# Kernel tuning notes

Measured on AMD Instinct MI355X. Metric: run time of the kernel, lower is better.

Reference implementation:

```python
import jax, jax.numpy as jnp
import numpy as np

N = 50000      # nodes
E = 800000     # edges
F_IN = 1284    # nfeat (hardcoded in module)
H = 128        # hidden_layers
NEG_SLOPE_ATT = 0.2   # PyG GATConv default
NEG_SLOPE_OUT = 0.01  # CustomLeakyReLU assumed default


def setup_inputs() -> dict:
    key = jax.random.key(0)
    ks = jax.random.split(key, 16)
    def glorot(k, shape):
        fan = sum(shape) if len(shape) > 1 else shape[0] + 1
        lim = np.sqrt(6.0 / fan).astype(np.float32)
        return jax.random.uniform(k, shape, jnp.float32, -lim, lim)
    x = jax.random.normal(ks[0], (N, F_IN), jnp.float32)
    edge_index = jax.random.randint(ks[1], (2, E), 0, N, jnp.int64)
    edge_attr = jax.random.uniform(ks[2], (E, 1), jnp.float32)
    return {
        'x': x, 'edge_index': edge_index, 'edge_attr': edge_attr,
        # conv1: 1284 -> 128, heads=1, edge_dim=1
        'W1': glorot(ks[3], (F_IN, H)),
        'att_src1': glorot(ks[4], (H,)),
        'att_dst1': glorot(ks[5], (H,)),
        'We1': glorot(ks[6], (1, H)),
        'att_e1': glorot(ks[7], (H,)),
        'b1': jnp.zeros((H,), jnp.float32),
        # conv2: 128 -> 1, heads=1, edge_dim=1
        'W2': glorot(ks[8], (H, 1)),
        'att_src2': glorot(ks[9], (1,)),
        'att_dst2': glorot(ks[10], (1,)),
        'We2': glorot(ks[11], (1, 1)),
        'att_e2': glorot(ks[12], (1,)),
        'b2': jnp.zeros((1,), jnp.float32),
    }


def _gat_layer(h_in, src, dst, eattr, W, a_src, a_dst, We, a_e, b):
    # h_in: [N, Fin]; src/dst: [E'] (with self-loops); eattr: [E', 1]
    h = h_in @ W                                   # [N, F]
    alpha_src = h @ a_src                          # [N]
    alpha_dst = h @ a_dst                          # [N]
    alpha_e = (eattr @ We) @ a_e                   # [E']
    alpha = alpha_src[src] + alpha_dst[dst] + alpha_e
    alpha = jax.nn.leaky_relu(alpha, NEG_SLOPE_ATT)
    # segment softmax over destination neighborhoods
    m = jax.ops.segment_max(alpha, dst, num_segments=N)
    ea = jnp.exp(alpha - m[dst])
    denom = jax.ops.segment_sum(ea, dst, num_segments=N)
    coef = ea / (denom[dst] + 1e-16)               # [E']
    out = jax.ops.segment_sum(coef[:, None] * h[src], dst, num_segments=N)
    return out + b


def reference(x, edge_index, edge_attr, W1, att_src1, att_dst1, We1, att_e1, b1,
              W2, att_src2, att_dst2, We2, att_e2, b2):
    # add self loops (PyG default, fill_value='mean' for edge_attr)
    loop = jnp.arange(N, dtype=edge_index.dtype)
    src = jnp.concatenate([edge_index[0], loop])
    dst = jnp.concatenate([edge_index[1], loop])
    loop_attr = jnp.broadcast_to(jnp.mean(edge_attr, axis=0, keepdims=True), (N, 1))
    eattr = jnp.concatenate([edge_attr, loop_attr], axis=0)

    x1 = _gat_layer(x, src, dst, eattr, W1, att_src1, att_dst1, We1, att_e1, b1)
    x2 = jax.nn.elu(x1)
    # dropout p=0.2 is identity in eval mode
    x4 = _gat_layer(x2, src, dst, eattr, W2, att_src2, att_dst2, We2, att_e2, b2)
    return jax.nn.leaky_relu(x4, NEG_SLOPE_OUT)  # [N, 1]
```

## Files before the change

kernel.cpp:

```cpp
#include <hip/hip_runtime.h>
#include <math.h>

#define NN 50000
#define NE 800000
#define NEP 850000
#define FI 1284
#define HD 128
#define KP 1312
#define NSTEP 41
#define NH (NN * HD)
#define PAD 64
#define NBLK ((NN + 255) / 256)
#define NROWB ((NN + 127) / 128)
#define WP_ELEMS (NSTEP * 4096)
#define WT_BLKS ((WP_ELEMS + 255) / 256)

typedef float f32x4 __attribute__((ext_vector_type(4)));
typedef short bfrag __attribute__((ext_vector_type(8)));


__device__ __forceinline__ float wave_reduce_sum(float v) {
    #pragma unroll
    for (int off = 32; off; off >>= 1) v += __shfl_down(v, off);
    return v;
}

__device__ __forceinline__ ushort f2bf(float f) {
    unsigned u = __float_as_uint(f);
    u += 0x7FFFu + ((u >> 16) & 1u);
    return (ushort)(u >> 16);
}

__device__ __forceinline__ float bf2f(ushort u) {
    return __uint_as_float(((unsigned)u) << 16);
}

__device__ __forceinline__ ushort f2h(float f) {
    _Float16 h = (_Float16)f;
    return *(ushort*)&h;
}

__device__ __forceinline__ float h2f(ushort u) {
    _Float16 h = *(_Float16*)&u;
    return (float)h;
}

__device__ __forceinline__ bfrag cvt_frag(float4 a0, float4 a1) {
    union { int i[4]; bfrag f; } u;
    asm("v_cvt_pk_bf16_f32 %0, %1, %2" : "=v"(u.i[0]) : "v"(a0.x), "v"(a0.y));
    asm("v_cvt_pk_bf16_f32 %0, %1, %2" : "=v"(u.i[1]) : "v"(a0.z), "v"(a0.w));
    asm("v_cvt_pk_bf16_f32 %0, %1, %2" : "=v"(u.i[2]) : "v"(a1.x), "v"(a1.y));
    asm("v_cvt_pk_bf16_f32 %0, %1, %2" : "=v"(u.i[3]) : "v"(a1.z), "v"(a1.w));
    return u.f;
}


__global__ __launch_bounds__(256) void k_pre_a(int* cursor, float* sc,
                                               const float* We1, const float* ae1,
                                               const float* We2, const float* ae2) {
    if (blockIdx.x < NBLK) {
        int i = blockIdx.x * 256 + threadIdx.x;
        if (i < NN) cursor[i] = i * PAD;
        if (i == 0) { sc[0] = 0.f; sc[3] = 0.f; sc[4] = 0.f; sc[5] = 0.f; sc[6] = 0.f; sc[7] = 0.f; }
    } else if (threadIdx.x < 64) {
        int l = threadIdx.x;
        float v = We1[l] * ae1[l] + We1[l + 64] * ae1[l + 64];
        v = wave_reduce_sum(v);
        if (l == 0) { sc[1] = v; sc[2] = We2[0] * ae2[0]; }
    }
}


__global__ __launch_bounds__(256) void k_pre_b(const float* __restrict__ W, ushort* __restrict__ Wp,
                                               const float* __restrict__ eattr, float* sc) {
    int b = blockIdx.x;
    if (b < WT_BLKS) {
        int i = b * 256 + threadIdx.x;
        if (i >= WP_ELEMS) return;
        int s = i >> 12;
        int r = i & 4095;
        int cg = r >> 9;
        int q = r & 511;
        int lane = q >> 3, j = q & 7;
        int k = s * 32 + (lane >> 4) * 8 + j;
        int c = cg * 16 + (lane & 15);
        float v = (k < FI) ? W[(size_t)k * HD + c] : 0.f;
        Wp[i] = f2bf(v);
    } else {
        __shared__ float wsum[4];
        int b2 = b - WT_BLKS;
        float v = 0.f;
        for (int i = b2 * 256 + threadIdx.x; i < NE; i += 256 * 256)
            v += eattr[i];
        v = wave_reduce_sum(v);
        int wid = threadIdx.x >> 6, l = threadIdx.x & 63;
        if (l == 0) wsum[wid] = v;
        __syncthreads();
        if (threadIdx.x == 0)
            atomicAdd(&sc[0], wsum[0] + wsum[1] + wsum[2] + wsum[3]);
    }
}


__global__ __launch_bounds__(512) void k_gemm1_mfma(const float* __restrict__ x,
                                                    const ushort* __restrict__ Wp,
                                                    ushort* __restrict__ h1,
                                                    const float* __restrict__ asrc,
                                                    const float* __restrict__ adst,
                                                    float* __restrict__ as1,
                                                    float* __restrict__ ad1) {
    __shared__ float  As[3][128][32];
    __shared__ ushort Bs[3][4096];
    const int t = threadIdx.x;
    const int wid = t >> 6, l = t & 63;
    const int lr = l & 15, lg = l >> 4;
    const int wrow0 = blockIdx.x * 128 + wid * 16;

    const int srow = l >> 3;
    const int schunk = (l & 7) ^ srow;
    int g0 = wrow0 + srow;      if (g0 > NN - 1) g0 = NN - 1;
    int g1 = wrow0 + 8 + srow;  if (g1 > NN - 1) g1 = NN - 1;
    const float* sp0 = x + (size_t)g0 * FI + schunk * 4;
    const float* sp1 = x + (size_t)g1 * FI + schunk * 4;

    const ushort* bq0 = Wp + wid * 512 + l * 8;

    const int rs0 = (lg * 2)     ^ (lr & 7);
    const int rs1 = (lg * 2 + 1) ^ (lr & 7);

    f32x4 acc[8];
    #pragma unroll
    for (int c = 0; c < 8; ++c) acc[c] = (f32x4){0.f, 0.f, 0.f, 0.f};

#define STAGE(B, IT) do { \
    __builtin_amdgcn_global_load_lds( \
        (const __attribute__((address_space(1))) unsigned int*)(sp0 + (size_t)(IT) * 32), \
        (__attribute__((address_space(3))) unsigned int*)&As[B][wid * 16][0], 16, 0, 0); \
    __builtin_amdgcn_global_load_lds( \
        (const __attribute__((address_space(1))) unsigned int*)(sp1 + (size_t)(IT) * 32), \
        (__attribute__((address_space(3))) unsigned int*)&As[B][wid * 16 + 8][0], 16, 0, 0); \
    __builtin_amdgcn_global_load_lds( \
        (const __attribute__((address_space(1))) unsigned int*)(bq0 + (size_t)(IT) * 4096), \
        (__attribute__((address_space(3))) unsigned int*)&Bs[B][wid * 512], 16, 0, 0); \
} while (0)

    STAGE(0, 0);
    STAGE(1, 1);
    STAGE(2, 2);
    asm volatile("s_waitcnt vmcnt(6)" ::: "memory");
    __builtin_amdgcn_s_barrier();

    int bsel = 0;
    for (int it = 0; it < 40; ++it) {
        bfrag bfr[8];
        #pragma unroll
        for (int cg = 0; cg < 8; ++cg)
            bfr[cg] = *(const bfrag*)&Bs[bsel][cg * 512 + l * 8];

        float4 a0 = *(const float4*)&As[bsel][wid * 16 + lr][rs0 * 4];
        float4 a1 = *(const float4*)&As[bsel][wid * 16 + lr][rs1 * 4];
        bfrag af = cvt_frag(a0, a1);
        #pragma unroll
        for (int cg = 0; cg < 8; ++cg)
            acc[cg] = __builtin_amdgcn_mfma_f32_16x16x32_bf16(af, bfr[cg], acc[cg], 0, 0, 0);

        __builtin_amdgcn_s_barrier();
        if (it + 3 < 40) {
            STAGE(bsel, it + 3);
            asm volatile("s_waitcnt vmcnt(6)" ::: "memory");
        } else if (it == 37) {
            asm volatile("s_waitcnt vmcnt(3)" ::: "memory");
        } else if (it == 38) {
            asm volatile("s_waitcnt vmcnt(0)" ::: "memory");
        }
        __builtin_amdgcn_s_barrier();
        bsel = (bsel == 2) ? 0 : bsel + 1;
    }
#undef STAGE

    {
        int rowc = wrow0 + lr; if (rowc > NN - 1) rowc = NN - 1;
        float4 a0t = make_float4(0.f, 0.f, 0.f, 0.f);
        if (lg == 0) a0t = *(const float4*)(x + (size_t)rowc * FI + 1280);
        bfrag af;
        af[0] = (short)f2bf(a0t.x); af[1] = (short)f2bf(a0t.y);
        af[2] = (short)f2bf(a0t.z); af[3] = (short)f2bf(a0t.w);
        af[4] = 0; af[5] = 0; af[6] = 0; af[7] = 0;
        const ushort* wqs = Wp + (size_t)40 * 4096 + l * 8;
        #pragma unroll
        for (int cg = 0; cg < 8; ++cg) {
            bfrag bf = *(const bfrag*)(wqs + cg * 512);
            acc[cg] = __builtin_amdgcn_mfma_f32_16x16x32_bf16(af, bf, acc[cg], 0, 0, 0);
        }
    }

    #pragma unroll
    for (int cg = 0; cg < 8; ++cg) {
        #pragma unroll
        for (int r = 0; r < 4; ++r) {
            int gr = wrow0 + lg * 4 + r;
            if (gr < NN) h1[(size_t)gr * HD + cg * 16 + lr] = f2bf(acc[cg][r]);
        }
    }

    float av[8], dv[8];
    #pragma unroll
    for (int cg = 0; cg < 8; ++cg) {
        av[cg] = asrc[cg * 16 + lr];
        dv[cg] = adst[cg * 16 + lr];
    }
    #pragma unroll
    for (int r = 0; r < 4; ++r) {
        float s = 0.f, d = 0.f;
        #pragma unroll
        for (int cg = 0; cg < 8; ++cg) {
            s += acc[cg][r] * av[cg];
            d += acc[cg][r] * dv[cg];
        }
        #pragma unroll
        for (int off = 1; off < 16; off <<= 1) {
            s += __shfl_xor(s, off);
            d += __shfl_xor(d, off);
        }
        int gr = wrow0 + lg * 4 + r;
        if (lr == 0 && gr < NN) { as1[gr] = s; ad1[gr] = d; }
    }
}


__global__ void k_place(const int* __restrict__ ei, const float* __restrict__ eattr,
                        const float* __restrict__ sc,
                        const float* __restrict__ as1, const float* __restrict__ ad1,
                        int* cursor, int2* __restrict__ csr) {
    int e = blockIdx.x * blockDim.x + threadIdx.x;
    if (e >= NEP) return;
    int s, d; float av;
    if (e < NE) { s = ei[e]; d = ei[NE + e]; av = eattr[e]; }
    else        { s = d = e - NE; av = sc[0] * (1.0f / NE); }
    float a = as1[s] + ad1[d] + sc[1] * av;
    a = (a > 0.f) ? a : 0.2f * a;
    int pos = atomicAdd(&cursor[d], 1);
    if (pos - d * PAD < PAD)
        csr[pos] = make_int2(s, ((int)f2h(a) << 16) | (int)f2h(av));
}


__global__ __launch_bounds__(256) void k_layer1(const int2* __restrict__ csr,
                                                const int* __restrict__ cursor,
                                                const ushort* __restrict__ h1,
                                                const float* __restrict__ b1,
                                                const float* __restrict__ W2,
                                                float* __restrict__ h2) {
    int wid = threadIdx.x >> 6, l = threadIdx.x & 63;
    int d = blockIdx.x * 4 + wid;
    if (d >= NN) return;
    int s0 = d * PAD;
    int n = cursor[d] - s0; if (n > PAD) n = PAD;

    float m = -INFINITY;
    for (int i = 0; i < n; ++i)
        m = fmaxf(m, h2f((ushort)(csr[s0 + i].y >> 16)));

    float den = 0.f, ax = 0.f, ay = 0.f;
    int i = 0;
    for (; i + 4 <= n; i += 4) {
        int2 e0 = csr[s0 + i],     e1 = csr[s0 + i + 1];
        int2 e2 = csr[s0 + i + 2], e3 = csr[s0 + i + 3];
        float w0 = expf(h2f((ushort)(e0.y >> 16)) - m);
        float w1 = expf(h2f((ushort)(e1.y >> 16)) - m);
        float w2 = expf(h2f((ushort)(e2.y >> 16)) - m);
        float w3 = expf(h2f((ushort)(e3.y >> 16)) - m);
        ushort2 hv0 = *(const ushort2*)&h1[(size_t)e0.x * HD + 2 * l];
        ushort2 hv1 = *(const ushort2*)&h1[(size_t)e1.x * HD + 2 * l];
        ushort2 hv2 = *(const ushort2*)&h1[(size_t)e2.x * HD + 2 * l];
        ushort2 hv3 = *(const ushort2*)&h1[(size_t)e3.x * HD + 2 * l];
        den += w0 + w1 + w2 + w3;
        ax += w0 * bf2f(hv0.x) + w1 * bf2f(hv1.x) + w2 * bf2f(hv2.x) + w3 * bf2f(hv3.x);
        ay += w0 * bf2f(hv0.y) + w1 * bf2f(hv1.y) + w2 * bf2f(hv2.y) + w3 * bf2f(hv3.y);
    }
    for (; i < n; ++i) {
        int2 e0 = csr[s0 + i];
        float w0 = expf(h2f((ushort)(e0.y >> 16)) - m);
        ushort2 hv0 = *(const ushort2*)&h1[(size_t)e0.x * HD + 2 * l];
        den += w0;
        ax += w0 * bf2f(hv0.x);
        ay += w0 * bf2f(hv0.y);
    }
    float inv = 1.f / (den + 1e-16f);
    ax *= inv; ay *= inv;
    float2 bb = *(const float2*)&b1[2 * l];
    float2 w  = *(const float2*)&W2[2 * l];
    float a = ax + bb.x; a = (a > 0.f) ? a : (expf(a) - 1.f);
    float b = ay + bb.y; b = (b > 0.f) ? b : (expf(b) - 1.f);
    float p = a * w.x + b * w.y;
    p = wave_reduce_sum(p);
    if (l == 0) h2[d] = p;
}


__global__ __launch_bounds__(256) void k_layer2(const int2* __restrict__ csr,
                                                const int* __restrict__ cursor,
                                                const float* __restrict__ h2,
                                                const float* __restrict__ as2,
                                                const float* __restrict__ ad2,
                                                const float* __restrict__ sc,
                                                const float* __restrict__ b2,
                                                float* __restrict__ out) {
    int d = blockIdx.x * blockDim.x + threadIdx.x;
    if (d >= NN) return;
    int s0 = d * PAD;
    int n = cursor[d] - s0; if (n > PAD) n = PAD;
    float A = as2[0], D = ad2[0], c2 = sc[2];
    float hd = D * h2[d];

    float m = -INFINITY;
    for (int i = 0; i < n; ++i) {
        int2 sa = csr[s0 + i];
        float a = A * h2[sa.x] + hd + c2 * h2f((ushort)(sa.y & 0xFFFF));
        a = (a > 0.f) ? a : 0.2f * a;
        m = fmaxf(m, a);
    }
    float den = 0.f, num = 0.f;
    for (int i = 0; i < n; ++i) {
        int2 sa = csr[s0 + i];
        float hs = h2[sa.x];
        float a = A * hs + hd + c2 * h2f((ushort)(sa.y & 0xFFFF));
        a = (a > 0.f) ? a : 0.2f * a;
        float wgt = expf(a - m);
        den += wgt;
        num += wgt * hs;
    }
    float v = num / (den + 1e-16f) + b2[0];
    out[d] = (v >= 0.f) ? v : 0.01f * v;
}


extern "C" void kernel_launch(void* const* d_in, const int* in_sizes, int n_in,
                              void* d_out, int out_size, void* d_ws, size_t ws_size,
                              hipStream_t stream) {
    const float* x     = (const float*)d_in[0];
    const int*   ei    = (const int*)d_in[1];
    const float* eattr = (const float*)d_in[2];
    const float* W1    = (const float*)d_in[3];
    const float* asrc1 = (const float*)d_in[4];
    const float* adst1 = (const float*)d_in[5];
    const float* We1   = (const float*)d_in[6];
    const float* ae1   = (const float*)d_in[7];
    const float* b1    = (const float*)d_in[8];
    const float* W2    = (const float*)d_in[9];
    const float* as2   = (const float*)d_in[10];
    const float* ad2   = (const float*)d_in[11];
    const float* We2   = (const float*)d_in[12];
    const float* ae2   = (const float*)d_in[13];
    const float* b2    = (const float*)d_in[14];
    float* out = (float*)d_out;

    ushort* h1  = (ushort*)d_ws;
    float* as1  = (float*)(h1 + (size_t)NH);
    float* ad1  = as1 + NN;
    float* h2   = ad1 + NN;
    float* sc   = h2 + NN;
    int*   cursor = (int*)(sc + 8);
    int2*  csr    = (int2*)(cursor + NN);
    ushort* Wp  = (ushort*)(csr + (size_t)NN * PAD);

    k_pre_a<<<NBLK + 1, 256, 0, stream>>>(cursor, sc, We1, ae1, We2, ae2);
    k_pre_b<<<WT_BLKS + 256, 256, 0, stream>>>(W1, Wp, eattr, sc);

    k_gemm1_mfma<<<NROWB, 512, 0, stream>>>(x, Wp, h1, asrc1, adst1, as1, ad1);

    k_place<<<(NEP + 255) / 256, 256, 0, stream>>>(ei, eattr, sc, as1, ad1, cursor, csr);

    k_layer1<<<(NN + 3) / 4, 256, 0, stream>>>(csr, cursor, h1, b1, W2, h2);
    k_layer2<<<(NN + 255) / 256, 256, 0, stream>>>(csr, cursor, h2, as2, ad2, sc, b2, out);
}
```

Baseline: 223.5 us.

## Merge preprocessing kernels and use online softmax in aggregation layers

The two preprocessing kernels become one launch. The edge-attribute sum is now written as per-block partials, and a single wave in the GEMM kernel reduces them, which removes the atomic and the separate zeroing. Both aggregation kernels switch from a two-pass max-then-sum softmax to a single-pass online softmax with rescaling, so each CSR segment is read once instead of twice. The cost is extra exp and rescale work whenever the running max grows, plus a small serial reduction at the start of GEMM block 0.

```diff
diff --git a/kernel.cpp b/kernel.cpp
--- a/kernel.cpp
+++ b/kernel.cpp
@@ -55,27 +55,24 @@
 }
 
 
-__global__ __launch_bounds__(256) void k_pre_a(int* cursor, float* sc,
-                                               const float* We1, const float* ae1,
-                                               const float* We2, const float* ae2) {
-    if (blockIdx.x < NBLK) {
-        int i = blockIdx.x * 256 + threadIdx.x;
+__global__ __launch_bounds__(256) void k_pre(int* cursor, float* sc,
+                                             const float* We1, const float* ae1,
+                                             const float* We2, const float* ae2,
+                                             const float* __restrict__ W, ushort* __restrict__ Wp,
+                                             const float* __restrict__ eattr, float* bsum) {
+    int b = blockIdx.x;
+    if (b < NBLK) {
+        int i = b * 256 + threadIdx.x;
         if (i < NN) cursor[i] = i * PAD;
-        if (i == 0) { sc[0] = 0.f; sc[3] = 0.f; sc[4] = 0.f; sc[5] = 0.f; sc[6] = 0.f; sc[7] = 0.f; }
-    } else if (threadIdx.x < 64) {
-        int l = threadIdx.x;
-        float v = We1[l] * ae1[l] + We1[l + 64] * ae1[l + 64];
-        v = wave_reduce_sum(v);
-        if (l == 0) { sc[1] = v; sc[2] = We2[0] * ae2[0]; }
-    }
-}
-
-
-__global__ __launch_bounds__(256) void k_pre_b(const float* __restrict__ W, ushort* __restrict__ Wp,
-                                               const float* __restrict__ eattr, float* sc) {
-    int b = blockIdx.x;
-    if (b < WT_BLKS) {
-        int i = b * 256 + threadIdx.x;
+    } else if (b == NBLK) {
+        if (threadIdx.x < 64) {
+            int l = threadIdx.x;
+            float v = We1[l] * ae1[l] + We1[l + 64] * ae1[l + 64];
+            v = wave_reduce_sum(v);
+            if (l == 0) { sc[1] = v; sc[2] = We2[0] * ae2[0]; }
+        }
+    } else if (b < NBLK + 1 + WT_BLKS) {
+        int i = (b - NBLK - 1) * 256 + threadIdx.x;
         if (i >= WP_ELEMS) return;
         int s = i >> 12;
         int r = i & 4095;
@@ -88,7 +85,7 @@
         Wp[i] = f2bf(v);
     } else {
         __shared__ float wsum[4];
-        int b2 = b - WT_BLKS;
+        int b2 = b - NBLK - 1 - WT_BLKS;
         float v = 0.f;
         for (int i = b2 * 256 + threadIdx.x; i < NE; i += 256 * 256)
             v += eattr[i];
@@ -97,7 +94,7 @@
         if (l == 0) wsum[wid] = v;
         __syncthreads();
         if (threadIdx.x == 0)
-            atomicAdd(&sc[0], wsum[0] + wsum[1] + wsum[2] + wsum[3]);
+            bsum[b2] = wsum[0] + wsum[1] + wsum[2] + wsum[3];
     }
 }
 
@@ -108,13 +105,21 @@
                                                     const float* __restrict__ asrc,
                                                     const float* __restrict__ adst,
                                                     float* __restrict__ as1,
-                                                    float* __restrict__ ad1) {
+                                                    float* __restrict__ ad1,
+                                                    const float* __restrict__ bsum,
+                                                    float* sc) {
     __shared__ float  As[3][128][32];
     __shared__ ushort Bs[3][4096];
     const int t = threadIdx.x;
     const int wid = t >> 6, l = t & 63;
     const int lr = l & 15, lg = l >> 4;
     const int wrow0 = blockIdx.x * 128 + wid * 16;
+
+    if (blockIdx.x == 0 && wid == 0) {
+        float v = bsum[l] + bsum[l + 64] + bsum[l + 128] + bsum[l + 192];
+        v = wave_reduce_sum(v);
+        if (l == 0) sc[0] = v;
+    }
 
     const int srow = l >> 3;
     const int schunk = (l & 7) ^ srow;
@@ -257,31 +262,39 @@
     int s0 = d * PAD;
     int n = cursor[d] - s0; if (n > PAD) n = PAD;
 
-    float m = -INFINITY;
-    for (int i = 0; i < n; ++i)
-        m = fmaxf(m, h2f((ushort)(csr[s0 + i].y >> 16)));
-
-    float den = 0.f, ax = 0.f, ay = 0.f;
+    float m = -INFINITY, den = 0.f, ax = 0.f, ay = 0.f;
     int i = 0;
     for (; i + 4 <= n; i += 4) {
         int2 e0 = csr[s0 + i],     e1 = csr[s0 + i + 1];
         int2 e2 = csr[s0 + i + 2], e3 = csr[s0 + i + 3];
-        float w0 = expf(h2f((ushort)(e0.y >> 16)) - m);
-        float w1 = expf(h2f((ushort)(e1.y >> 16)) - m);
-        float w2 = expf(h2f((ushort)(e2.y >> 16)) - m);
-        float w3 = expf(h2f((ushort)(e3.y >> 16)) - m);
+        float a0 = h2f((ushort)(e0.y >> 16));
+        float a1 = h2f((ushort)(e1.y >> 16));
+        float a2 = h2f((ushort)(e2.y >> 16));
+        float a3 = h2f((ushort)(e3.y >> 16));
         ushort2 hv0 = *(const ushort2*)&h1[(size_t)e0.x * HD + 2 * l];
         ushort2 hv1 = *(const ushort2*)&h1[(size_t)e1.x * HD + 2 * l];
         ushort2 hv2 = *(const ushort2*)&h1[(size_t)e2.x * HD + 2 * l];
         ushort2 hv3 = *(const ushort2*)&h1[(size_t)e3.x * HD + 2 * l];
+        float mt = fmaxf(fmaxf(a0, a1), fmaxf(a2, a3));
+        if (mt > m) {
+            float r = expf(m - mt);
+            den *= r; ax *= r; ay *= r; m = mt;
+        }
+        float w0 = expf(a0 - m), w1 = expf(a1 - m);
+        float w2 = expf(a2 - m), w3 = expf(a3 - m);
         den += w0 + w1 + w2 + w3;
         ax += w0 * bf2f(hv0.x) + w1 * bf2f(hv1.x) + w2 * bf2f(hv2.x) + w3 * bf2f(hv3.x);
         ay += w0 * bf2f(hv0.y) + w1 * bf2f(hv1.y) + w2 * bf2f(hv2.y) + w3 * bf2f(hv3.y);
     }
     for (; i < n; ++i) {
         int2 e0 = csr[s0 + i];
-        float w0 = expf(h2f((ushort)(e0.y >> 16)) - m);
+        float a0 = h2f((ushort)(e0.y >> 16));
         ushort2 hv0 = *(const ushort2*)&h1[(size_t)e0.x * HD + 2 * l];
+        if (a0 > m) {
+            float r = expf(m - a0);
+            den *= r; ax *= r; ay *= r; m = a0;
+        }
+        float w0 = expf(a0 - m);
         den += w0;
         ax += w0 * bf2f(hv0.x);
         ay += w0 * bf2f(hv0.y);
@@ -313,19 +326,39 @@
     float A = as2[0], D = ad2[0], c2 = sc[2];
     float hd = D * h2[d];
 
-    float m = -INFINITY;
-    for (int i = 0; i < n; ++i) {
-        int2 sa = csr[s0 + i];
-        float a = A * h2[sa.x] + hd + c2 * h2f((ushort)(sa.y & 0xFFFF));
-        a = (a > 0.f) ? a : 0.2f * a;
-        m = fmaxf(m, a);
-    }
-    float den = 0.f, num = 0.f;
-    for (int i = 0; i < n; ++i) {
+    float m = -INFINITY, den = 0.f, num = 0.f;
+    int i = 0;
+    for (; i + 4 <= n; i += 4) {
+        int2 s_0 = csr[s0 + i],     s_1 = csr[s0 + i + 1];
+        int2 s_2 = csr[s0 + i + 2], s_3 = csr[s0 + i + 3];
+        float h0 = h2[s_0.x], h1v = h2[s_1.x], h2v = h2[s_2.x], h3 = h2[s_3.x];
+        float a0 = A * h0 + hd + c2 * h2f((ushort)(s_0.y & 0xFFFF));
+        float a1 = A * h1v + hd + c2 * h2f((ushort)(s_1.y & 0xFFFF));
+        float a2 = A * h2v + hd + c2 * h2f((ushort)(s_2.y & 0xFFFF));
+        float a3 = A * h3 + hd + c2 * h2f((ushort)(s_3.y & 0xFFFF));
+        a0 = (a0 > 0.f) ? a0 : 0.2f * a0;
+        a1 = (a1 > 0.f) ? a1 : 0.2f * a1;
+        a2 = (a2 > 0.f) ? a2 : 0.2f * a2;
+        a3 = (a3 > 0.f) ? a3 : 0.2f * a3;
+        float mt = fmaxf(fmaxf(a0, a1), fmaxf(a2, a3));
+        if (mt > m) {
+            float r = expf(m - mt);
+            den *= r; num *= r; m = mt;
+        }
+        float w0 = expf(a0 - m), w1 = expf(a1 - m);
+        float w2 = expf(a2 - m), w3 = expf(a3 - m);
+        den += w0 + w1 + w2 + w3;
+        num += w0 * h0 + w1 * h1v + w2 * h2v + w3 * h3;
+    }
+    for (; i < n; ++i) {
         int2 sa = csr[s0 + i];
         float hs = h2[sa.x];
         float a = A * hs + hd + c2 * h2f((ushort)(sa.y & 0xFFFF));
         a = (a > 0.f) ? a : 0.2f * a;
+        if (a > m) {
+            float r = expf(m - a);
+            den *= r; num *= r; m = a;
+        }
         float wgt = expf(a - m);
         den += wgt;
         num += wgt * hs;
@@ -360,14 +393,15 @@
     float* ad1  = as1 + NN;
     float* h2   = ad1 + NN;
     float* sc   = h2 + NN;
-    int*   cursor = (int*)(sc + 8);
+    float* bsum = sc + 8;
+    int*   cursor = (int*)(bsum + 256);
     int2*  csr    = (int2*)(cursor + NN);
     ushort* Wp  = (ushort*)(csr + (size_t)NN * PAD);
 
-    k_pre_a<<<NBLK + 1, 256, 0, stream>>>(cursor, sc, We1, ae1, We2, ae2);
-    k_pre_b<<<WT_BLKS + 256, 256, 0, stream>>>(W1, Wp, eattr, sc);
-
-    k_gemm1_mfma<<<NROWB, 512, 0, stream>>>(x, Wp, h1, asrc1, adst1, as1, ad1);
+    k_pre<<<NBLK + 1 + WT_BLKS + 256, 256, 0, stream>>>(cursor, sc, We1, ae1, We2, ae2,
+                                                        W1, Wp, eattr, bsum);
+
+    k_gemm1_mfma<<<NROWB, 512, 0, stream>>>(x, Wp, h1, asrc1, adst1, as1, ad1, bsum, sc);
 
     k_place<<<(NEP + 255) / 256, 256, 0, stream>>>(ei, eattr, sc, as1, ad1, cursor, csr);
 
```

After: 182.7 us, median of 2. 1.22x faster.
